# Kernel optimization log

Measured on AMD Instinct MI355X. Metric: run time of the kernel, lower is better.

## Reference

```python
import jax, jax.numpy as jnp
import numpy as np

IN_DIM, DIM, G, B = 512, 1024, 16, 4096

def _gelu(x):
    return jax.nn.gelu(x, approximate=False)  # torch nn.GELU default = exact erf


def setup_inputs() -> dict:
    key = jax.random.key(0)
    ks = jax.random.split(key, 11)
    sc_in = 1.0 / np.sqrt(IN_DIM)
    sc_d = 1.0 / np.sqrt(DIM)
    return {
        "x": jax.random.normal(ks[0], (B, IN_DIM), dtype=jnp.float32),
        "genre": jax.random.randint(ks[1], (B,), 0, G),
        # shared MLP params
        "W1": jax.random.uniform(ks[2], (IN_DIM, DIM), jnp.float32, -sc_in, sc_in),
        "b1": jax.random.uniform(ks[3], (DIM,), jnp.float32, -sc_in, sc_in),
        "W2": jax.random.uniform(ks[4], (DIM, DIM), jnp.float32, -sc_d, sc_d),
        "b2": jax.random.uniform(ks[5], (DIM,), jnp.float32, -sc_d, sc_d),
        # unshared (per-genre) MLP params, stacked over experts
        "Wa": jax.random.uniform(ks[6], (G, DIM, DIM), jnp.float32, -sc_d, sc_d),
        "ba": jax.random.uniform(ks[7], (G, DIM), jnp.float32, -sc_d, sc_d),
        "Wb": jax.random.uniform(ks[8], (G, DIM, DIM), jnp.float32, -sc_d, sc_d),
        "bb": jax.random.uniform(ks[9], (G, DIM), jnp.float32, -sc_d, sc_d),
    }


def reference(x, genre, W1, b1, W2, b2, Wa, ba, Wb, bb):
    # shared trunk: Linear -> GELU -> Linear -> GELU
    s = _gelu(_gelu(x @ W1 + b1) @ W2 + b2)          # [B, D]
    # dense per-genre expert branches (faithful to original: compute all, then gather)
    h = _gelu(jnp.einsum('bd,gde->bge', s, Wa) + ba[None, :, :])  # [B, G, D]
    out_all = jnp.einsum('bgd,gde->bge', h, Wb) + bb[None, :, :]  # [B, G, D]
    # gather each sample's own genre branch
    return jnp.take_along_axis(out_all, genre[:, None, None], axis=1)[:, 0, :]  # [B, D]
```

## Files before the change

kernel.cpp:

```cpp
#include <hip/hip_runtime.h>
#include <hip/hip_bf16.h>
#include <math.h>

#define BATCH 4096
#define INDIM 512
#define NDIM  1024
#define NG    16

typedef __bf16 bf16_t;
typedef __bf16 bf16x8 __attribute__((ext_vector_type(8)));
typedef float  f32x4  __attribute__((ext_vector_type(4)));
typedef unsigned int u32;
typedef unsigned int u32x4 __attribute__((ext_vector_type(4)));

__device__ __forceinline__ float gelu_exact(float v) {
    return 0.5f * v * (1.0f + erff(v * 0.70710678118654752440f));
}

__device__ __forceinline__ void gload_lds16(const void* g, void* l) {
    __builtin_amdgcn_global_load_lds((const __attribute__((address_space(1))) void*)g,
                                     (__attribute__((address_space(3))) void*)l,
                                     16, 0, 0);
}

__device__ __forceinline__ u32 pkbf(float a, float b) {
    union { bf16_t h[2]; u32 v; } x;
    x.h[0] = (bf16_t)a; x.h[1] = (bf16_t)b;
    return x.v;
}

template<int N> __device__ __forceinline__ void waitvm() {
    if constexpr (N == 0)       asm volatile("s_waitcnt vmcnt(0)"  ::: "memory");
    else if constexpr (N == 2)  asm volatile("s_waitcnt vmcnt(2)"  ::: "memory");
    else if constexpr (N == 4)  asm volatile("s_waitcnt vmcnt(4)"  ::: "memory");
    else if constexpr (N == 8)  asm volatile("s_waitcnt vmcnt(8)"  ::: "memory");
    else                        asm volatile("s_waitcnt vmcnt(10)" ::: "memory");
}

template<int NT>
__device__ __forceinline__ void strip_body(const float* __restrict__ src,
                                           bf16_t* __restrict__ dst,
                                           int N, int K, int n0, int kbase,
                                           int t, u32* __restrict__ Tsh) {
    const int kp_l = t >> 4;
    const int nc   = (t & 15) * 4;
    const int kr0  = kp_l * 2;
    const int n    = t >> 2;
    const int c4   = (t & 3) * 4;

    f32x4 r[3][4];

    auto load = [&](int slot, int kt) {
        const float* p = src + (size_t)(kbase + kt * 64 + kr0) * N + n0 + nc;
        r[slot][0] = *(const f32x4*)p;
        r[slot][1] = *(const f32x4*)(p + N);
        r[slot][2] = *(const f32x4*)(p + 32 * N);
        r[slot][3] = *(const f32x4*)(p + 33 * N);
        __builtin_amdgcn_sched_barrier(0);
    };
    auto pack = [&](int slot, int buf) {
        u32* Tb = Tsh + buf * (64 * 34);
        Tb[(nc + 0) * 34 + kp_l]      = pkbf(r[slot][0][0], r[slot][1][0]);
        Tb[(nc + 1) * 34 + kp_l]      = pkbf(r[slot][0][1], r[slot][1][1]);
        Tb[(nc + 2) * 34 + kp_l]      = pkbf(r[slot][0][2], r[slot][1][2]);
        Tb[(nc + 3) * 34 + kp_l]      = pkbf(r[slot][0][3], r[slot][1][3]);
        Tb[(nc + 0) * 34 + 16 + kp_l] = pkbf(r[slot][2][0], r[slot][3][0]);
        Tb[(nc + 1) * 34 + 16 + kp_l] = pkbf(r[slot][2][1], r[slot][3][1]);
        Tb[(nc + 2) * 34 + 16 + kp_l] = pkbf(r[slot][2][2], r[slot][3][2]);
        Tb[(nc + 3) * 34 + 16 + kp_l] = pkbf(r[slot][2][3], r[slot][3][3]);
    };
    auto flush = [&](int buf, int kt) {
        u32* Tb = Tsh + buf * (64 * 34);
        u32 v[8];
        #pragma unroll
        for (int j = 0; j < 4; ++j) v[j]     = Tb[n * 34 + c4 + j];
        #pragma unroll
        for (int j = 0; j < 4; ++j) v[4 + j] = Tb[n * 34 + 16 + c4 + j];
        u32* d = (u32*)((char*)dst + ((size_t)(n0 + n) * K + kbase + kt * 64) * 2);
        *(u32x4*)(d + c4)      = (u32x4){v[0], v[1], v[2], v[3]};
        *(u32x4*)(d + 16 + c4) = (u32x4){v[4], v[5], v[6], v[7]};
    };

    load(0, 0);
    if constexpr (NT > 1) load(1, 1);
    #pragma unroll
    for (int kt = 0; kt < NT; ++kt) {
        if (kt + 2 < NT) load((kt + 2) % 3, kt + 2);
        if (kt + 2 < NT) {
            if (kt == 0) waitvm<8>(); else waitvm<10>();
        } else if (kt + 1 < NT) {
            if (kt == 0) waitvm<4>(); else waitvm<8>();
        } else {
            if (kt == 0) waitvm<0>();
            else if (kt == 1) waitvm<2>();
            else waitvm<4>();
        }
        pack(kt % 3, kt & 1);
        asm volatile("s_waitcnt lgkmcnt(0)" ::: "memory");
        asm volatile("s_barrier" ::: "memory");
        flush(kt & 1, kt);
    }
}

#define PREP_CVT_BLOCKS 1024
#define PREP_W1_GROUPS  64
#define PREP_W2_GROUPS  64
__global__ __launch_bounds__(256)
void prep_kernel(const int* __restrict__ genre, int* __restrict__ perm,
                 int* __restrict__ offsets,
                 const float* __restrict__ x, bf16_t* __restrict__ xb,
                 const float* __restrict__ W1, bf16_t* __restrict__ W1t,
                 const float* __restrict__ W2, bf16_t* __restrict__ W2t) {
    __shared__ char smem[17408];
    const int bx = blockIdx.x;
    const int t  = threadIdx.x;

    if (bx == 0) {
        int (*cc)[NG] = (int(*)[NG])smem;
        int* gtot = (int*)(smem + 4096);
        int* goff = (int*)(smem + 4096 + 256);
        for (int i = t; i < 64 * NG; i += 256) (&cc[0][0])[i] = 0;
        __syncthreads();
        if (t < 64) {
            #pragma unroll 1
            for (int i = 0; i < 64; ++i) {
                int g = genre[t * 64 + i] & (NG - 1);
                cc[t][g] += 1;
            }
        }
        __syncthreads();
        if (t < NG) {
            int s = 0;
            #pragma unroll 1
            for (int c = 0; c < 64; ++c) { int v = cc[c][t]; cc[c][t] = s; s += v; }
            gtot[t] = s;
        }
        __syncthreads();
        if (t == 0) {
            int s = 0;
            for (int g = 0; g < NG; ++g) { goff[g] = s; offsets[g] = s; s += gtot[g]; }
            offsets[NG] = s;
        }
        __syncthreads();
        if (t < 64) {
            #pragma unroll 1
            for (int i = 0; i < 64; ++i) {
                int b = t * 64 + i;
                int g = genre[b] & (NG - 1);
                int pos = goff[g] + cc[t][g];
                cc[t][g] += 1;
                perm[pos] = b;
            }
        }
    } else if (bx < 1 + PREP_CVT_BLOCKS) {
        const int i = ((bx - 1) * 256 + t) * 8;
        float4 a = *(const float4*)&x[i];
        float4 b = *(const float4*)&x[i + 4];
        bf16x8 w;
        w[0] = (bf16_t)a.x; w[1] = (bf16_t)a.y; w[2] = (bf16_t)a.z; w[3] = (bf16_t)a.w;
        w[4] = (bf16_t)b.x; w[5] = (bf16_t)b.y; w[6] = (bf16_t)b.z; w[7] = (bf16_t)b.w;
        *(bf16x8*)&xb[i] = w;
    } else if (bx < 1 + PREP_CVT_BLOCKS + PREP_W1_GROUPS) {
        const int gid  = bx - 1 - PREP_CVT_BLOCKS;
        const int band = gid >> 2, ksl = gid & 3;
        strip_body<INDIM / 256>(W1, W1t, NDIM, INDIM, band * 64, ksl * (INDIM / 4),
                                t, (u32*)smem);
    } else {
        const int gid  = bx - 1 - PREP_CVT_BLOCKS - PREP_W1_GROUPS;
        const int band = gid >> 2, ksl = gid & 3;
        strip_body<NDIM / 256>(W2, W2t, NDIM, NDIM, band * 64, ksl * (NDIM / 4),
                               t, (u32*)smem);
    }
}

__global__ __launch_bounds__(256)
void transpose_strip2_kernel(const float* __restrict__ srcA, bf16_t* __restrict__ dstA,
                             const float* __restrict__ srcB, bf16_t* __restrict__ dstB) {
    __shared__ u32 T[2 * 64 * 34];
    const int z = blockIdx.z;
    const size_t slab = (size_t)(z & 15) * NDIM * NDIM;
    const float* s = (z < 16 ? srcA : srcB) + slab;
    bf16_t*      d = (z < 16 ? dstA : dstB) + slab;
    strip_body<NDIM / 256>(s, d, NDIM, NDIM, blockIdx.x * 64,
                           blockIdx.y * (NDIM / 4), threadIdx.x, T);
}

template<bool EXPERT, bool GATHER_A, bool GELU_OUT, bool SCATTER_OUT, bool OUT_BF16>
__global__ __launch_bounds__(1024, 4)
void gemm128_kernel(const bf16_t* __restrict__ A,
                    const bf16_t* __restrict__ Bt,
                    const float* __restrict__ bias,
                    void* __restrict__ Cout,
                    int K,
                    const int* __restrict__ perm,
                    const int* __restrict__ offsets) {
    constexpr int N = NDIM;
    __shared__ bf16_t As[2][128 * 64];
    __shared__ bf16_t Bs[2][128 * 64];

    const int n0 = blockIdx.y * 128;
    int m0 = 0, mloc0 = 0, count = 1 << 30, gbase = 0;
    const bf16_t* Bp = Bt;
    const float* biasp = bias;

    if constexpr (EXPERT) {
        const int bx = blockIdx.x;
        int g = 0, accum = 0, cnt = 0;
        for (; g < NG; ++g) {
            cnt = offsets[g + 1] - offsets[g];
            int nt = (cnt + 127) >> 7;
            if (bx < accum + nt) break;
            accum += nt;
        }
        if (g >= NG) return;
        count = cnt;
        mloc0 = (bx - accum) * 128;
        gbase = offsets[g];
        m0 = gbase + mloc0;
        Bp = Bt + (size_t)g * N * NDIM;
        biasp = bias + g * N;
    } else {
        m0 = blockIdx.x * 128;
    }

    const int tid  = threadIdx.x;
    const int wave = tid >> 6;
    const int lane = tid & 63;
    const int l15  = lane & 15;
    const int l16  = lane >> 4;
    const int wr   = wave >> 2;
    const int wc   = wave & 3;

    const int srow   = tid >> 3;
    const int srcoff = (((tid & 7) ^ ((tid >> 3) & 7)) * 16);
    int arow;
    if constexpr (EXPERT) {
        int rcl = mloc0 + srow;
        if (rcl >= count) rcl = count - 1;
        arow = GATHER_A ? perm[gbase + rcl] : (gbase + rcl);
    } else {
        arow = m0 + srow;
    }
    const char* aptr = (const char*)(A + (size_t)arow * K) + srcoff;
    const char* bptr = (const char*)(Bp + (size_t)(n0 + srow) * K) + srcoff;

    f32x4 acc[2][2];
    #pragma unroll
    for (int m = 0; m < 2; ++m)
        #pragma unroll
        for (int n = 0; n < 2; ++n)
            acc[m][n] = (f32x4){0.f, 0.f, 0.f, 0.f};

    const int nsteps = K >> 6;
    const int w1024 = wave * 1024;

    auto stage = [&](int buf, int t) {
        const size_t ko = (size_t)t * 128;
        gload_lds16(aptr + ko, (char*)&As[buf][0] + w1024);
        gload_lds16(bptr + ko, (char*)&Bs[buf][0] + w1024);
    };

    stage(0, 0);
    int cur = 0;
    for (int t = 0; t < nsteps; ++t) {
        if (t + 1 < nsteps) {
            stage(cur ^ 1, t + 1);
            asm volatile("s_waitcnt vmcnt(2)" ::: "memory");
        } else {
            asm volatile("s_waitcnt vmcnt(0)" ::: "memory");
        }
        asm volatile("s_barrier" ::: "memory");

        #pragma unroll
        for (int kk = 0; kk < 2; ++kk) {
            bf16x8 a[2], b[2];
            #pragma unroll
            for (int m = 0; m < 2; ++m) {
                const int row = wr * 32 + m * 16 + l15;
                const int chunk = (kk * 4 + l16) ^ (lane & 7);
                a[m] = *(const bf16x8*)&As[cur][row * 64 + chunk * 8];
            }
            #pragma unroll
            for (int n = 0; n < 2; ++n) {
                const int row = wc * 32 + n * 16 + l15;
                const int chunk = (kk * 4 + l16) ^ (lane & 7);
                b[n] = *(const bf16x8*)&Bs[cur][row * 64 + chunk * 8];
            }
            #pragma unroll
            for (int m = 0; m < 2; ++m)
                #pragma unroll
                for (int n = 0; n < 2; ++n)
                    acc[m][n] = __builtin_amdgcn_mfma_f32_16x16x32_bf16(a[m], b[n], acc[m][n], 0, 0, 0);
        }
        asm volatile("s_barrier" ::: "memory");
        cur ^= 1;
    }

    #pragma unroll
    for (int n = 0; n < 2; ++n) {
        const int col = n0 + wc * 32 + n * 16 + l15;
        const float bv = biasp[col];
        #pragma unroll
        for (int m = 0; m < 2; ++m) {
            #pragma unroll
            for (int r = 0; r < 4; ++r) {
                const int row_local = wr * 32 + m * 16 + l16 * 4 + r;
                if constexpr (EXPERT) {
                    if (mloc0 + row_local >= count) continue;
                }
                float v = acc[m][n][r] + bv;
                if constexpr (GELU_OUT) v = gelu_exact(v);
                int orow = m0 + row_local;
                if constexpr (SCATTER_OUT) orow = perm[orow];
                if constexpr (OUT_BF16)
                    ((bf16_t*)Cout)[(size_t)orow * N + col] = (bf16_t)v;
                else
                    ((float*)Cout)[(size_t)orow * N + col] = v;
            }
        }
    }
}

extern "C" void kernel_launch(void* const* d_in, const int* in_sizes, int n_in,
                              void* d_out, int out_size, void* d_ws, size_t ws_size,
                              hipStream_t stream) {
    const float* x     = (const float*)d_in[0];
    const int*   genre = (const int*)  d_in[1];
    const float* W1    = (const float*)d_in[2];
    const float* b1    = (const float*)d_in[3];
    const float* W2    = (const float*)d_in[4];
    const float* b2    = (const float*)d_in[5];
    const float* Wa    = (const float*)d_in[6];
    const float* ba    = (const float*)d_in[7];
    const float* Wb    = (const float*)d_in[8];
    const float* bb    = (const float*)d_in[9];
    float* out = (float*)d_out;

    char* ws = (char*)d_ws;
    const size_t MB = 1 << 20;
    bf16_t* W1t = (bf16_t*)(ws);
    bf16_t* W2t = (bf16_t*)(ws + 1 * MB);
    bf16_t* Wat = (bf16_t*)(ws + 3 * MB);
    bf16_t* Wbt = (bf16_t*)(ws + 35 * MB);
    bf16_t* xb  = (bf16_t*)(ws + 67 * MB);
    bf16_t* s1b = (bf16_t*)(ws + 71 * MB);
    bf16_t* sb  = (bf16_t*)(ws + 79 * MB);
    int*    perm    = (int*)(ws + 87 * MB);
    int*    offsets = (int*)(ws + 87 * MB + 65536);
    bf16_t* hb = s1b;

    prep_kernel<<<1 + PREP_CVT_BLOCKS + PREP_W1_GROUPS + PREP_W2_GROUPS, 256, 0, stream>>>(
        genre, perm, offsets, x, xb, W1, W1t, W2, W2t);
    transpose_strip2_kernel<<<dim3(NDIM / 64, 4, 2 * NG), 256, 0, stream>>>(
        Wa, Wat, Wb, Wbt);
    gemm128_kernel<false, false, true, false, true><<<dim3(32, 8), 1024, 0, stream>>>(
        xb, W1t, b1, s1b, INDIM, nullptr, nullptr);
    gemm128_kernel<false, false, true, false, true><<<dim3(32, 8), 1024, 0, stream>>>(
        s1b, W2t, b2, sb, NDIM, nullptr, nullptr);
    gemm128_kernel<true, true, true, false, true><<<dim3(48, 8), 1024, 0, stream>>>(
        sb, Wat, ba, hb, NDIM, perm, offsets);
    gemm128_kernel<true, false, false, true, false><<<dim3(48, 8), 1024, 0, stream>>>(
        hb, Wbt, bb, out, NDIM, perm, offsets);
}
```

Baseline: 137.3 us.

## Fuse expert weight transposes into trunk GEMM launches to overlap work

```diff
diff --git a/kernel.cpp b/kernel.cpp
--- a/kernel.cpp
+++ b/kernel.cpp
@@ -11,6 +11,7 @@
 typedef __bf16 bf16x8 __attribute__((ext_vector_type(8)));
 typedef float  f32x4  __attribute__((ext_vector_type(4)));
 typedef unsigned int u32;
+typedef unsigned int u32x2 __attribute__((ext_vector_type(2)));
 typedef unsigned int u32x4 __attribute__((ext_vector_type(4)));
 
 __device__ __forceinline__ float gelu_exact(float v) {
@@ -173,19 +174,145 @@
     }
 }
 
-__global__ __launch_bounds__(256)
-void transpose_strip2_kernel(const float* __restrict__ srcA, bf16_t* __restrict__ dstA,
-                             const float* __restrict__ srcB, bf16_t* __restrict__ dstB) {
-    __shared__ u32 T[2 * 64 * 34];
-    const int z = blockIdx.z;
-    const size_t slab = (size_t)(z & 15) * NDIM * NDIM;
-    const float* s = (z < 16 ? srcA : srcB) + slab;
-    bf16_t*      d = (z < 16 ? dstA : dstB) + slab;
-    strip_body<NDIM / 256>(s, d, NDIM, NDIM, blockIdx.x * 64,
-                           blockIdx.y * (NDIM / 4), threadIdx.x, T);
-}
-
-template<bool EXPERT, bool GATHER_A, bool GELU_OUT, bool SCATTER_OUT, bool OUT_BF16>
+__device__ __forceinline__ void tr1024_body(const float* __restrict__ src,
+                                            bf16_t* __restrict__ dst,
+                                            int n0, char* smem) {
+    float* T = (float*)smem;
+    const int t   = threadIdx.x;
+    const int row = t >> 4;
+    const int nc  = (t & 15) * 4;
+    const int n   = t >> 4;
+    const int kq  = t & 15;
+
+    f32x4 reg = *(const f32x4*)(src + (size_t)row * NDIM + n0 + nc);
+    #pragma unroll 1
+    for (int kt = 0; kt < 16; ++kt) {
+        float* Tb = T + (kt & 1) * (64 * 71);
+        *(f32x4*)&Tb[row * 71 + nc] = reg;
+        if (kt + 1 < 16)
+            reg = *(const f32x4*)(src + (size_t)((kt + 1) * 64 + row) * NDIM + n0 + nc);
+        __syncthreads();
+        const float f0 = Tb[(kq * 4 + 0) * 71 + n];
+        const float f1 = Tb[(kq * 4 + 1) * 71 + n];
+        const float f2 = Tb[(kq * 4 + 2) * 71 + n];
+        const float f3 = Tb[(kq * 4 + 3) * 71 + n];
+        u32x2 v;
+        v.x = pkbf(f0, f1);
+        v.y = pkbf(f2, f3);
+        *(u32x2*)((u32*)((char*)dst + ((size_t)(n0 + n) * NDIM + kt * 64) * 2) + kq * 2) = v;
+        __syncthreads();
+    }
+}
+
+__device__ __forceinline__ void trunk1024_body(const bf16_t* __restrict__ A,
+                                               const bf16_t* __restrict__ Bt,
+                                               const float* __restrict__ bias,
+                                               bf16_t* __restrict__ Cout,
+                                               int K, int m0, int n0, char* smem) {
+    constexpr int N = NDIM;
+    char* As = smem;
+    char* Bs = smem + 32768;
+
+    const int tid  = threadIdx.x;
+    const int wave = tid >> 6;
+    const int lane = tid & 63;
+    const int l15  = lane & 15;
+    const int l16  = lane >> 4;
+    const int wr   = wave >> 2;
+    const int wc   = wave & 3;
+
+    const int srow   = tid >> 3;
+    const int srcoff = (((tid & 7) ^ ((tid >> 3) & 7)) * 16);
+    const char* aptr = (const char*)(A + (size_t)(m0 + srow) * K) + srcoff;
+    const char* bptr = (const char*)(Bt + (size_t)(n0 + srow) * K) + srcoff;
+
+    f32x4 acc[2][2];
+    #pragma unroll
+    for (int m = 0; m < 2; ++m)
+        #pragma unroll
+        for (int n = 0; n < 2; ++n)
+            acc[m][n] = (f32x4){0.f, 0.f, 0.f, 0.f};
+
+    const int nsteps = K >> 6;
+    const int w1024 = wave * 1024;
+
+    auto stage = [&](int buf, int t) {
+        const size_t ko = (size_t)t * 128;
+        gload_lds16(aptr + ko, As + buf * 16384 + w1024);
+        gload_lds16(bptr + ko, Bs + buf * 16384 + w1024);
+    };
+
+    stage(0, 0);
+    int cur = 0;
+    for (int t = 0; t < nsteps; ++t) {
+        if (t + 1 < nsteps) {
+            stage(cur ^ 1, t + 1);
+            asm volatile("s_waitcnt vmcnt(2)" ::: "memory");
+        } else {
+            asm volatile("s_waitcnt vmcnt(0)" ::: "memory");
+        }
+        asm volatile("s_barrier" ::: "memory");
+
+        #pragma unroll
+        for (int kk = 0; kk < 2; ++kk) {
+            bf16x8 a[2], b[2];
+            #pragma unroll
+            for (int m = 0; m < 2; ++m) {
+                const int row = wr * 32 + m * 16 + l15;
+                const int chunk = (kk * 4 + l16) ^ (lane & 7);
+                a[m] = *(const bf16x8*)(As + cur * 16384 + (row * 64 + chunk * 8) * 2);
+            }
+            #pragma unroll
+            for (int n = 0; n < 2; ++n) {
+                const int row = wc * 32 + n * 16 + l15;
+                const int chunk = (kk * 4 + l16) ^ (lane & 7);
+                b[n] = *(const bf16x8*)(Bs + cur * 16384 + (row * 64 + chunk * 8) * 2);
+            }
+            #pragma unroll
+            for (int m = 0; m < 2; ++m)
+                #pragma unroll
+                for (int n = 0; n < 2; ++n)
+                    acc[m][n] = __builtin_amdgcn_mfma_f32_16x16x32_bf16(a[m], b[n], acc[m][n], 0, 0, 0);
+        }
+        asm volatile("s_barrier" ::: "memory");
+        cur ^= 1;
+    }
+
+    #pragma unroll
+    for (int n = 0; n < 2; ++n) {
+        const int col = n0 + wc * 32 + n * 16 + l15;
+        const float bv = bias[col];
+        #pragma unroll
+        for (int m = 0; m < 2; ++m) {
+            #pragma unroll
+            for (int r = 0; r < 4; ++r) {
+                const int row_local = wr * 32 + m * 16 + l16 * 4 + r;
+                float v = gelu_exact(acc[m][n][r] + bv);
+                Cout[(size_t)(m0 + row_local) * N + col] = (bf16_t)v;
+            }
+        }
+    }
+}
+
+__global__ __launch_bounds__(1024, 2)
+void fused_kernel(const bf16_t* __restrict__ A, const bf16_t* __restrict__ Bt,
+                  const float* __restrict__ bias, bf16_t* __restrict__ Cout, int K,
+                  const float* __restrict__ Wsrc, bf16_t* __restrict__ Wdst) {
+    __shared__ char smem[65536];
+    const int bx = blockIdx.x;
+    if (bx & 1) {
+        const int sid  = bx >> 1;
+        const int slab = sid >> 4;
+        const int band = sid & 15;
+        tr1024_body(Wsrc + (size_t)slab * NDIM * NDIM,
+                    Wdst + (size_t)slab * NDIM * NDIM, band * 64, smem);
+    } else {
+        const int gid = bx >> 1;
+        trunk1024_body(A, Bt, bias, Cout, K, (gid & 31) * 128, (gid >> 5) * 128, smem);
+    }
+}
+
+template<bool GATHER_A, bool GELU_OUT, bool SCATTER_OUT, bool OUT_BF16>
 __global__ __launch_bounds__(1024, 4)
 void gemm128_kernel(const bf16_t* __restrict__ A,
                     const bf16_t* __restrict__ Bt,
@@ -203,7 +330,7 @@
     const bf16_t* Bp = Bt;
     const float* biasp = bias;
 
-    if constexpr (EXPERT) {
+    {
         const int bx = blockIdx.x;
         int g = 0, accum = 0, cnt = 0;
         for (; g < NG; ++g) {
@@ -219,8 +346,6 @@
         m0 = gbase + mloc0;
         Bp = Bt + (size_t)g * N * NDIM;
         biasp = bias + g * N;
-    } else {
-        m0 = blockIdx.x * 128;
     }
 
     const int tid  = threadIdx.x;
@@ -234,12 +359,10 @@
     const int srow   = tid >> 3;
     const int srcoff = (((tid & 7) ^ ((tid >> 3) & 7)) * 16);
     int arow;
-    if constexpr (EXPERT) {
+    {
         int rcl = mloc0 + srow;
         if (rcl >= count) rcl = count - 1;
         arow = GATHER_A ? perm[gbase + rcl] : (gbase + rcl);
-    } else {
-        arow = m0 + srow;
     }
     const char* aptr = (const char*)(A + (size_t)arow * K) + srcoff;
     const char* bptr = (const char*)(Bp + (size_t)(n0 + srow) * K) + srcoff;
@@ -305,9 +428,7 @@
             #pragma unroll
             for (int r = 0; r < 4; ++r) {
                 const int row_local = wr * 32 + m * 16 + l16 * 4 + r;
-                if constexpr (EXPERT) {
-                    if (mloc0 + row_local >= count) continue;
-                }
+                if (mloc0 + row_local >= count) continue;
                 float v = acc[m][n][r] + bv;
                 if constexpr (GELU_OUT) v = gelu_exact(v);
                 int orow = m0 + row_local;
@@ -351,14 +472,10 @@
 
     prep_kernel<<<1 + PREP_CVT_BLOCKS + PREP_W1_GROUPS + PREP_W2_GROUPS, 256, 0, stream>>>(
         genre, perm, offsets, x, xb, W1, W1t, W2, W2t);
-    transpose_strip2_kernel<<<dim3(NDIM / 64, 4, 2 * NG), 256, 0, stream>>>(
-        Wa, Wat, Wb, Wbt);
-    gemm128_kernel<false, false, true, false, true><<<dim3(32, 8), 1024, 0, stream>>>(
-        xb, W1t, b1, s1b, INDIM, nullptr, nullptr);
-    gemm128_kernel<false, false, true, false, true><<<dim3(32, 8), 1024, 0, stream>>>(
-        s1b, W2t, b2, sb, NDIM, nullptr, nullptr);
-    gemm128_kernel<true, true, true, false, true><<<dim3(48, 8), 1024, 0, stream>>>(
+    fused_kernel<<<512, 1024, 0, stream>>>(xb, W1t, b1, s1b, INDIM, Wa, Wat);
+    fused_kernel<<<512, 1024, 0, stream>>>(s1b, W2t, b2, sb, NDIM, Wb, Wbt);
+    gemm128_kernel<true, true, false, true><<<dim3(48, 8), 1024, 0, stream>>>(
         sb, Wat, ba, hb, NDIM, perm, offsets);
-    gemm128_kernel<true, false, false, true, false><<<dim3(48, 8), 1024, 0, stream>>>(
+    gemm128_kernel<false, false, true, false><<<dim3(48, 8), 1024, 0, stream>>>(
         hb, Wbt, bb, out, NDIM, perm, offsets);
 }
```

Measured after the change: 122.2 us. -11.0%, faster.
